# Kernel tuning notes

Hardware: AMD Instinct MI355X
Metric: run time of the kernel (lower is better)

## Reference

```python
import jax, jax.numpy as jnp
import numpy as np

N = 6144
INPUT_SIZE = 1024
HIDDEN = 256
NEG_INF = -9e15  # matches torch masked_fill value -9000000000000000.0


def setup_inputs() -> dict:
    key = jax.random.key(0)
    k1, k2, k3, k4 = jax.random.split(key, 4)
    nodes_embed = jax.random.normal(k1, (N, INPUT_SIZE), dtype=jnp.float32)
    node_adj = jax.random.randint(k2, (N, N), 0, 2, dtype=jnp.int32)
    # learned params (xavier-uniform-ish scaling)
    limW = np.sqrt(6.0 / (INPUT_SIZE + HIDDEN))
    W = jax.random.uniform(k3, (INPUT_SIZE, HIDDEN), minval=-limW, maxval=limW, dtype=jnp.float32)
    lima = 1.414 * np.sqrt(6.0 / (2 * HIDDEN + 1))
    a_edge = jax.random.uniform(k4, (2 * HIDDEN,), minval=-lima, maxval=lima, dtype=jnp.float32)
    return {"nodes_embed": nodes_embed, "W": W, "a_edge": a_edge, "node_adj": node_adj}


def reference(nodes_embed, W, a_edge, node_adj):
    # h = nodes_embed @ W : [N, hidden]
    h = nodes_embed @ W
    # W_edge([h_i ; h_j]) decomposes exactly: (h_i @ a1) + (h_j @ a2)
    a1, a2 = a_edge[:HIDDEN], a_edge[HIDDEN:]
    score = (h @ a1)[:, None] + (h @ a2)[None, :]  # [N, N]
    adj_f = node_adj.astype(h.dtype)
    weight = jax.nn.leaky_relu(adj_f * score, negative_slope=0.2)
    weight = jnp.where(node_adj == 0, jnp.asarray(NEG_INF, h.dtype), weight)
    attention = jax.nn.softmax(weight, axis=-1)
    # dropout in eval mode (identity)
    return attention @ h  # [N, hidden]
```

## Files before the change

### kernel.cpp

```cpp
#include <hip/hip_runtime.h>
#include <hip/hip_bf16.h>

#define NN 6144
#define INPUT 1024
#define HID 256

using frag  = __attribute__((ext_vector_type(8))) short;
using f32x4 = __attribute__((ext_vector_type(4))) float;

static __device__ __forceinline__ unsigned short bf16u(float x) {
    unsigned u = __float_as_uint(x);
    u += 0x7fff + ((u >> 16) & 1);
    return (unsigned short)(u >> 16);
}

static __device__ __forceinline__ void gll16(const void* g, void* l) {
    __builtin_amdgcn_global_load_lds((__attribute__((address_space(1))) const void*)g,
                                     (__attribute__((address_space(3))) void*)l, 16, 0, 0);
}
static __device__ __forceinline__ void gll4(const void* g, void* l) {
    __builtin_amdgcn_global_load_lds((__attribute__((address_space(1))) const void*)g,
                                     (__attribute__((address_space(3))) void*)l, 4, 0, 0);
}

static __device__ __forceinline__ void lds_barrier() {
    asm volatile("s_waitcnt lgkmcnt(0)" ::: "memory");
    __builtin_amdgcn_s_barrier();
    __builtin_amdgcn_sched_barrier(0);
}


__global__ __launch_bounds__(256) void k_prep(const float* __restrict__ X,
                                              const float* __restrict__ W,
                                              unsigned short* __restrict__ Xbp,
                                              unsigned short* __restrict__ Wtp) {
    int b = blockIdx.x;
    if (b < 3072) {
        int t = b * 256 + threadIdx.x;
        int i = t >> 7, k8 = t & 127;
        const float4* p = reinterpret_cast<const float4*>(X + (size_t)i * INPUT + k8 * 8);
        float4 x0 = p[0], x1 = p[1];
        frag v;
        v[0] = (short)bf16u(x0.x); v[1] = (short)bf16u(x0.y);
        v[2] = (short)bf16u(x0.z); v[3] = (short)bf16u(x0.w);
        v[4] = (short)bf16u(x1.x); v[5] = (short)bf16u(x1.y);
        v[6] = (short)bf16u(x1.z); v[7] = (short)bf16u(x1.w);
        size_t off = ((size_t)((i >> 4) * 32 + (k8 >> 2))) * 512 + (k8 & 3) * 128 + (i & 15) * 8;
        *reinterpret_cast<frag*>(Xbp + off) = v;
    } else {
        int u = (b - 3072) * 256 + threadIdx.x;
        int n = u >> 7, k8 = u & 127;
        int k = k8 * 8;
        frag v;
#pragma unroll
        for (int e = 0; e < 8; e++) v[e] = (short)bf16u(W[(size_t)(k + e) * HID + n]);
        size_t off = ((size_t)((n >> 4) * 32 + (k8 >> 2))) * 512 + (k8 & 3) * 128 + (n & 15) * 8;
        *reinterpret_cast<frag*>(Wtp + off) = v;
    }
}

__global__ __launch_bounds__(256, 4) void k_gemm1(const unsigned short* __restrict__ Xbp,
                                                  const unsigned short* __restrict__ Wtp,
                                                  const float* __restrict__ a_edge,
                                                  unsigned short* __restrict__ hTp,
                                                  float* __restrict__ s1,
                                                  float* __restrict__ s2) {
    int t = threadIdx.x;
    int w = t >> 6, l = t & 63, lm = l & 15, q = l >> 4;
    int bx = blockIdx.x, by = blockIdx.y;
    int i0 = bx * 32;
    int tn = by * 4 + w;

    const unsigned short* pA0 = Xbp + (size_t)(bx * 2) * 32 * 512 + l * 8;
    const unsigned short* pA1 = Xbp + (size_t)(bx * 2 + 1) * 32 * 512 + l * 8;
    const unsigned short* pB  = Wtp + (size_t)tn * 32 * 512 + l * 8;

    f32x4 acc0 = {}, acc1 = {};
    frag a0s[3], a1s[3], bs[3];
#pragma unroll
    for (int s = 0; s < 2; s++) {
        a0s[s] = *reinterpret_cast<const frag*>(pA0 + s * 512);
        a1s[s] = *reinterpret_cast<const frag*>(pA1 + s * 512);
        bs[s]  = *reinterpret_cast<const frag*>(pB  + s * 512);
    }
#pragma unroll
    for (int tk = 0; tk < 32; tk++) {
        int cur = tk % 3;
        if (tk < 30) {
            int nx = (tk + 2) % 3;
            a0s[nx] = *reinterpret_cast<const frag*>(pA0 + (tk + 2) * 512);
            a1s[nx] = *reinterpret_cast<const frag*>(pA1 + (tk + 2) * 512);
            bs[nx]  = *reinterpret_cast<const frag*>(pB  + (tk + 2) * 512);
        }
        acc0 = __builtin_amdgcn_mfma_f32_16x16x32_bf16(a0s[cur], bs[cur], acc0, 0, 0, 0);
        acc1 = __builtin_amdgcn_mfma_f32_16x16x32_bf16(a1s[cur], bs[cur], acc1, 0, 0, 0);
    }

    unsigned short* tb = hTp + ((size_t)bx * 16 + tn) * 512;
    ushort4 o;
    o.x = bf16u(acc0[0]); o.y = bf16u(acc0[1]); o.z = bf16u(acc0[2]); o.w = bf16u(acc0[3]);
    *reinterpret_cast<ushort4*>(tb + (q >> 1) * 128 + lm * 8 + (q & 1) * 4) = o;
    o.x = bf16u(acc1[0]); o.y = bf16u(acc1[1]); o.z = bf16u(acc1[2]); o.w = bf16u(acc1[3]);
    *reinterpret_cast<ushort4*>(tb + (2 + (q >> 1)) * 128 + lm * 8 + (q & 1) * 4) = o;

    float a1v = a_edge[tn * 16 + lm], a2v = a_edge[HID + tn * 16 + lm];
#pragma unroll
    for (int h = 0; h < 2; h++) {
        const f32x4& ac = h ? acc1 : acc0;
#pragma unroll
        for (int r = 0; r < 4; r++) {
            float v1 = ac[r] * a1v, v2 = ac[r] * a2v;
            v1 += __shfl_xor(v1, 1); v2 += __shfl_xor(v2, 1);
            v1 += __shfl_xor(v1, 2); v2 += __shfl_xor(v2, 2);
            v1 += __shfl_xor(v1, 4); v2 += __shfl_xor(v2, 4);
            v1 += __shfl_xor(v1, 8); v2 += __shfl_xor(v2, 8);
            if (lm == 0) {
                atomicAdd(&s1[i0 + h * 16 + q * 4 + r], v1);
                atomicAdd(&s2[i0 + h * 16 + q * 4 + r], v2);
            }
        }
    }
}

__global__ __launch_bounds__(512, 2) void k_attn(const int* __restrict__ adj,
                                                 const float* __restrict__ s1,
                                                 const float* __restrict__ s2,
                                                 const unsigned short* __restrict__ hTp,
                                                 float* __restrict__ U4,
                                                 float* __restrict__ denom4) {
    __shared__ unsigned short P[2][32][136];
    __shared__ int   adjS[2][32][128];
    __shared__ float s2S[2][128];
    int t = threadIdx.x;
    int m = t >> 4, cg = t & 15;
    int i0 = blockIdx.x * 32;
    int q4 = blockIdx.y, j0 = q4 * 1536;
    int w = t >> 6, l = t & 63, lm = l & 15, q = l >> 4;

    float s1v = s1[i0 + m];
    const int*   astage = adj + (size_t)(i0 + w * 4 + (l >> 5)) * NN + j0 + (l & 31) * 4;
    const float* sstage = s2 + j0 + w * 16 + l;

    const unsigned short* hb = hTp + (size_t)(w * 2) * 512 + l * 8;
    int tjb = q4 * 48;

    f32x4 acc[2][2] = {};
    float dsum = 0.f;

#define STAGE(JC, BUF) { \
        gll16(astage + (JC), &adjS[BUF][w * 4][0]); \
        gll16(astage + (JC) + 2 * NN, &adjS[BUF][w * 4 + 2][0]); \
        if (l < 16) gll4(sstage + (JC), &s2S[BUF][w * 16]); }

    STAGE(0, 0)

    for (int c = 0; c < 12; c++) {
        int buf = c & 1, jc = c * 128;

        frag bf[8];
#pragma unroll
        for (int kk = 0; kk < 4; kk++)
#pragma unroll
            for (int nt = 0; nt < 2; nt++)
                bf[kk * 2 + nt] = *reinterpret_cast<const frag*>(
                    hb + ((size_t)(tjb + c * 4 + kk) * 16 + nt) * 512);

        asm volatile("s_waitcnt vmcnt(8)" ::: "memory");
        __builtin_amdgcn_s_barrier();
        __builtin_amdgcn_sched_barrier(0);
        if (c < 11) STAGE(jc + 128, buf ^ 1)

        {
            const int*   aL = &adjS[buf][m][cg * 8];
            const float* sL = &s2S[buf][cg * 8];
            int4   av0 = *reinterpret_cast<const int4*>(aL);
            int4   av1 = *reinterpret_cast<const int4*>(aL + 4);
            float4 sv0 = *reinterpret_cast<const float4*>(sL);
            float4 sv1 = *reinterpret_cast<const float4*>(sL + 4);
            float sc, wv, p0, p1, p2, p3, p4, p5, p6, p7;
            sc = s1v + sv0.x; wv = fmaxf(sc, 0.2f * sc); p0 = av0.x ? __expf(wv) : 0.f;
            sc = s1v + sv0.y; wv = fmaxf(sc, 0.2f * sc); p1 = av0.y ? __expf(wv) : 0.f;
            sc = s1v + sv0.z; wv = fmaxf(sc, 0.2f * sc); p2 = av0.z ? __expf(wv) : 0.f;
            sc = s1v + sv0.w; wv = fmaxf(sc, 0.2f * sc); p3 = av0.w ? __expf(wv) : 0.f;
            sc = s1v + sv1.x; wv = fmaxf(sc, 0.2f * sc); p4 = av1.x ? __expf(wv) : 0.f;
            sc = s1v + sv1.y; wv = fmaxf(sc, 0.2f * sc); p5 = av1.y ? __expf(wv) : 0.f;
            sc = s1v + sv1.z; wv = fmaxf(sc, 0.2f * sc); p6 = av1.z ? __expf(wv) : 0.f;
            sc = s1v + sv1.w; wv = fmaxf(sc, 0.2f * sc); p7 = av1.w ? __expf(wv) : 0.f;
            dsum += ((p0 + p1) + (p2 + p3)) + ((p4 + p5) + (p6 + p7));
            frag pk;
            pk[0] = (short)bf16u(p0); pk[1] = (short)bf16u(p1);
            pk[2] = (short)bf16u(p2); pk[3] = (short)bf16u(p3);
            pk[4] = (short)bf16u(p4); pk[5] = (short)bf16u(p5);
            pk[6] = (short)bf16u(p6); pk[7] = (short)bf16u(p7);
            *reinterpret_cast<frag*>(&P[buf][m][cg * 8]) = pk;
        }

        lds_barrier();

        __builtin_amdgcn_s_setprio(1);
#pragma unroll
        for (int kk = 0; kk < 4; kk++) {
            frag a0 = *reinterpret_cast<const frag*>(&P[buf][lm][kk * 32 + q * 8]);
            frag a1 = *reinterpret_cast<const frag*>(&P[buf][16 + lm][kk * 32 + q * 8]);
#pragma unroll
            for (int nt = 0; nt < 2; nt++) {
                acc[0][nt] = __builtin_amdgcn_mfma_f32_16x16x32_bf16(a0, bf[kk * 2 + nt], acc[0][nt], 0, 0, 0);
                acc[1][nt] = __builtin_amdgcn_mfma_f32_16x16x32_bf16(a1, bf[kk * 2 + nt], acc[1][nt], 0, 0, 0);
            }
        }
        __builtin_amdgcn_s_setprio(0);
    }
#undef STAGE

    float v = dsum;
    v += __shfl_xor(v, 1); v += __shfl_xor(v, 2);
    v += __shfl_xor(v, 4); v += __shfl_xor(v, 8);
    if (cg == 0) denom4[(size_t)q4 * NN + i0 + m] = v;

    float* Ub = U4 + (size_t)q4 * NN * HID;
#pragma unroll
    for (int h = 0; h < 2; h++)
#pragma unroll
        for (int nt = 0; nt < 2; nt++)
#pragma unroll
            for (int r = 0; r < 4; r++)
                Ub[(size_t)(i0 + h * 16 + q * 4 + r) * HID + w * 32 + nt * 16 + lm] = acc[h][nt][r];
}

__global__ __launch_bounds__(256) void k_norm(const float* __restrict__ U4,
                                              const float* __restrict__ denom4,
                                              float* __restrict__ out) {
    int i = blockIdx.x, t = threadIdx.x;
    size_t S = (size_t)NN * HID;
    size_t base = (size_t)i * HID + t;
    float u = U4[base] + U4[base + S] + U4[base + 2 * S] + U4[base + 3 * S];
    float d = denom4[i] + denom4[i + NN] + denom4[i + 2 * NN] + denom4[i + 3 * NN];
    out[base] = (d != 0.f) ? u / d : 0.f;
}

extern "C" void kernel_launch(void* const* d_in, const int* in_sizes, int n_in,
                              void* d_out, int out_size, void* d_ws, size_t ws_size,
                              hipStream_t stream) {
    const float* X      = (const float*)d_in[0];
    const float* W      = (const float*)d_in[1];
    const float* a_edge = (const float*)d_in[2];
    const int*   adj    = (const int*)d_in[3];
    float* out = (float*)d_out;

    float* U4     = (float*)d_ws;
    float* denom4 = U4 + (size_t)4 * NN * HID;
    float* s1     = denom4 + (size_t)4 * NN;
    float* s2     = s1 + NN;
    unsigned short* hTp = (unsigned short*)(s2 + NN);
    unsigned short* Wtp = hTp + (size_t)HID * NN;
    unsigned short* Xbp = (unsigned short*)U4;

    hipMemsetAsync(s1, 0, 2 * NN * sizeof(float), stream);
    k_prep<<<3072 + 128, 256, 0, stream>>>(X, W, Xbp, Wtp);
    k_gemm1<<<dim3(NN / 32, 4), 256, 0, stream>>>(Xbp, Wtp, a_edge, hTp, s1, s2);
    k_attn<<<dim3(NN / 32, 4), 512, 0, stream>>>(adj, s1, s2, hTp, U4, denom4);
    k_norm<<<NN, 256, 0, stream>>>(U4, denom4, out);
}
```

Measured before the change: 290.4 us.

## Compute attention probabilities directly in MFMA register fragments, dropping LDS staging

The attention kernel no longer stages adjacency and s2 through LDS or writes P to shared memory. Each lane loads the adjacency and s2 values it needs straight into registers, builds the bf16 B fragment with v_cvt_pk_bf16_f32, and runs the MFMAs with h^T as the A operand. This removes barriers and LDS traffic, and the block shrinks to 256 threads with 3 blocks per CU. Partial outputs are stored in fragment-tiled layout, and the normalization kernel transposes them through LDS and writes float4. The cost is uncoalesced 32-byte adjacency loads per lane with no explicit prefetch pipeline.

```diff
diff --git a/kernel.cpp b/kernel.cpp
--- a/kernel.cpp
+++ b/kernel.cpp
@@ -7,6 +7,8 @@
 
 using frag  = __attribute__((ext_vector_type(8))) short;
 using f32x4 = __attribute__((ext_vector_type(4))) float;
+
+union FU { frag f; unsigned u[4]; };
 
 static __device__ __forceinline__ unsigned short bf16u(float x) {
     unsigned u = __float_as_uint(x);
@@ -14,19 +16,10 @@
     return (unsigned short)(u >> 16);
 }
 
-static __device__ __forceinline__ void gll16(const void* g, void* l) {
-    __builtin_amdgcn_global_load_lds((__attribute__((address_space(1))) const void*)g,
-                                     (__attribute__((address_space(3))) void*)l, 16, 0, 0);
-}
-static __device__ __forceinline__ void gll4(const void* g, void* l) {
-    __builtin_amdgcn_global_load_lds((__attribute__((address_space(1))) const void*)g,
-                                     (__attribute__((address_space(3))) void*)l, 4, 0, 0);
-}
-
-static __device__ __forceinline__ void lds_barrier() {
-    asm volatile("s_waitcnt lgkmcnt(0)" ::: "memory");
-    __builtin_amdgcn_s_barrier();
-    __builtin_amdgcn_sched_barrier(0);
+static __device__ __forceinline__ unsigned cvtpk(float lo, float hi) {
+    unsigned r;
+    asm("v_cvt_pk_bf16_f32 %0, %1, %2" : "=v"(r) : "v"(lo), "v"(hi));
+    return r;
 }
 
 
@@ -122,120 +115,123 @@
     }
 }
 
-__global__ __launch_bounds__(512, 2) void k_attn(const int* __restrict__ adj,
+__global__ __launch_bounds__(256, 3) void k_attn(const int* __restrict__ adj,
                                                  const float* __restrict__ s1,
                                                  const float* __restrict__ s2,
                                                  const unsigned short* __restrict__ hTp,
-                                                 float* __restrict__ U4,
+                                                 float* __restrict__ U4p,
                                                  float* __restrict__ denom4) {
-    __shared__ unsigned short P[2][32][136];
-    __shared__ int   adjS[2][32][128];
-    __shared__ float s2S[2][128];
     int t = threadIdx.x;
-    int m = t >> 4, cg = t & 15;
-    int i0 = blockIdx.x * 32;
+    int w = t >> 6, l = t & 63, lm = l & 15, q = l >> 4;
+    int bx = blockIdx.x, i0 = bx * 32;
     int q4 = blockIdx.y, j0 = q4 * 1536;
-    int w = t >> 6, l = t & 63, lm = l & 15, q = l >> 4;
-
-    float s1v = s1[i0 + m];
-    const int*   astage = adj + (size_t)(i0 + w * 4 + (l >> 5)) * NN + j0 + (l & 31) * 4;
-    const float* sstage = s2 + j0 + w * 16 + l;
-
-    const unsigned short* hb = hTp + (size_t)(w * 2) * 512 + l * 8;
-    int tjb = q4 * 48;
-
-    f32x4 acc[2][2] = {};
-    float dsum = 0.f;
-
-#define STAGE(JC, BUF) { \
-        gll16(astage + (JC), &adjS[BUF][w * 4][0]); \
-        gll16(astage + (JC) + 2 * NN, &adjS[BUF][w * 4 + 2][0]); \
-        if (l < 16) gll4(sstage + (JC), &s2S[BUF][w * 16]); }
-
-    STAGE(0, 0)
-
-    for (int c = 0; c < 12; c++) {
-        int buf = c & 1, jc = c * 128;
-
-        frag bf[8];
-#pragma unroll
-        for (int kk = 0; kk < 4; kk++)
-#pragma unroll
-            for (int nt = 0; nt < 2; nt++)
-                bf[kk * 2 + nt] = *reinterpret_cast<const frag*>(
-                    hb + ((size_t)(tjb + c * 4 + kk) * 16 + nt) * 512);
-
-        asm volatile("s_waitcnt vmcnt(8)" ::: "memory");
-        __builtin_amdgcn_s_barrier();
-        __builtin_amdgcn_sched_barrier(0);
-        if (c < 11) STAGE(jc + 128, buf ^ 1)
-
-        {
-            const int*   aL = &adjS[buf][m][cg * 8];
-            const float* sL = &s2S[buf][cg * 8];
-            int4   av0 = *reinterpret_cast<const int4*>(aL);
-            int4   av1 = *reinterpret_cast<const int4*>(aL + 4);
-            float4 sv0 = *reinterpret_cast<const float4*>(sL);
-            float4 sv1 = *reinterpret_cast<const float4*>(sL + 4);
-            float sc, wv, p0, p1, p2, p3, p4, p5, p6, p7;
-            sc = s1v + sv0.x; wv = fmaxf(sc, 0.2f * sc); p0 = av0.x ? __expf(wv) : 0.f;
-            sc = s1v + sv0.y; wv = fmaxf(sc, 0.2f * sc); p1 = av0.y ? __expf(wv) : 0.f;
-            sc = s1v + sv0.z; wv = fmaxf(sc, 0.2f * sc); p2 = av0.z ? __expf(wv) : 0.f;
-            sc = s1v + sv0.w; wv = fmaxf(sc, 0.2f * sc); p3 = av0.w ? __expf(wv) : 0.f;
-            sc = s1v + sv1.x; wv = fmaxf(sc, 0.2f * sc); p4 = av1.x ? __expf(wv) : 0.f;
-            sc = s1v + sv1.y; wv = fmaxf(sc, 0.2f * sc); p5 = av1.y ? __expf(wv) : 0.f;
-            sc = s1v + sv1.z; wv = fmaxf(sc, 0.2f * sc); p6 = av1.z ? __expf(wv) : 0.f;
-            sc = s1v + sv1.w; wv = fmaxf(sc, 0.2f * sc); p7 = av1.w ? __expf(wv) : 0.f;
-            dsum += ((p0 + p1) + (p2 + p3)) + ((p4 + p5) + (p6 + p7));
-            frag pk;
-            pk[0] = (short)bf16u(p0); pk[1] = (short)bf16u(p1);
-            pk[2] = (short)bf16u(p2); pk[3] = (short)bf16u(p3);
-            pk[4] = (short)bf16u(p4); pk[5] = (short)bf16u(p5);
-            pk[6] = (short)bf16u(p6); pk[7] = (short)bf16u(p7);
-            *reinterpret_cast<frag*>(&P[buf][m][cg * 8]) = pk;
+
+    float s1a = s1[i0 + lm], s1b = s1[i0 + 16 + lm];
+    const int*   aL = adj + (size_t)(i0 + lm) * NN + j0 + q * 8;
+    const int*   aH = aL + (size_t)16 * NN;
+    const float* sp = s2 + j0 + q * 8;
+    const unsigned short* Ab = hTp + ((size_t)(q4 * 48) * 16 + w * 4) * 512 + l * 8;
+
+    f32x4 accL[4] = {}, accH[4] = {};
+    float dsL = 0.f, dsH = 0.f;
+
+#pragma unroll 2
+    for (int st = 0; st < 48; st++) {
+        const unsigned short* Abs = Ab + (size_t)st * 16 * 512;
+        frag A0 = *reinterpret_cast<const frag*>(Abs);
+        frag A1 = *reinterpret_cast<const frag*>(Abs + 512);
+        frag A2 = *reinterpret_cast<const frag*>(Abs + 1024);
+        frag A3 = *reinterpret_cast<const frag*>(Abs + 1536);
+        int4   al0 = *reinterpret_cast<const int4*>(aL + st * 32);
+        int4   al1 = *reinterpret_cast<const int4*>(aL + st * 32 + 4);
+        int4   ah0 = *reinterpret_cast<const int4*>(aH + st * 32);
+        int4   ah1 = *reinterpret_cast<const int4*>(aH + st * 32 + 4);
+        float4 sv0 = *reinterpret_cast<const float4*>(sp + st * 32);
+        float4 sv1 = *reinterpret_cast<const float4*>(sp + st * 32 + 4);
+
+        float sc, wv, p0, p1, p2, p3, p4, p5, p6, p7;
+        FU b0, b1;
+        sc = s1a + sv0.x; wv = fmaxf(sc, 0.2f * sc); p0 = al0.x ? __expf(wv) : 0.f;
+        sc = s1a + sv0.y; wv = fmaxf(sc, 0.2f * sc); p1 = al0.y ? __expf(wv) : 0.f;
+        sc = s1a + sv0.z; wv = fmaxf(sc, 0.2f * sc); p2 = al0.z ? __expf(wv) : 0.f;
+        sc = s1a + sv0.w; wv = fmaxf(sc, 0.2f * sc); p3 = al0.w ? __expf(wv) : 0.f;
+        sc = s1a + sv1.x; wv = fmaxf(sc, 0.2f * sc); p4 = al1.x ? __expf(wv) : 0.f;
+        sc = s1a + sv1.y; wv = fmaxf(sc, 0.2f * sc); p5 = al1.y ? __expf(wv) : 0.f;
+        sc = s1a + sv1.z; wv = fmaxf(sc, 0.2f * sc); p6 = al1.z ? __expf(wv) : 0.f;
+        sc = s1a + sv1.w; wv = fmaxf(sc, 0.2f * sc); p7 = al1.w ? __expf(wv) : 0.f;
+        dsL += ((p0 + p1) + (p2 + p3)) + ((p4 + p5) + (p6 + p7));
+        b0.u[0] = cvtpk(p0, p1); b0.u[1] = cvtpk(p2, p3);
+        b0.u[2] = cvtpk(p4, p5); b0.u[3] = cvtpk(p6, p7);
+        sc = s1b + sv0.x; wv = fmaxf(sc, 0.2f * sc); p0 = ah0.x ? __expf(wv) : 0.f;
+        sc = s1b + sv0.y; wv = fmaxf(sc, 0.2f * sc); p1 = ah0.y ? __expf(wv) : 0.f;
+        sc = s1b + sv0.z; wv = fmaxf(sc, 0.2f * sc); p2 = ah0.z ? __expf(wv) : 0.f;
+        sc = s1b + sv0.w; wv = fmaxf(sc, 0.2f * sc); p3 = ah0.w ? __expf(wv) : 0.f;
+        sc = s1b + sv1.x; wv = fmaxf(sc, 0.2f * sc); p4 = ah1.x ? __expf(wv) : 0.f;
+        sc = s1b + sv1.y; wv = fmaxf(sc, 0.2f * sc); p5 = ah1.y ? __expf(wv) : 0.f;
+        sc = s1b + sv1.z; wv = fmaxf(sc, 0.2f * sc); p6 = ah1.z ? __expf(wv) : 0.f;
+        sc = s1b + sv1.w; wv = fmaxf(sc, 0.2f * sc); p7 = ah1.w ? __expf(wv) : 0.f;
+        dsH += ((p0 + p1) + (p2 + p3)) + ((p4 + p5) + (p6 + p7));
+        b1.u[0] = cvtpk(p0, p1); b1.u[1] = cvtpk(p2, p3);
+        b1.u[2] = cvtpk(p4, p5); b1.u[3] = cvtpk(p6, p7);
+
+        __builtin_amdgcn_s_setprio(1);
+        accL[0] = __builtin_amdgcn_mfma_f32_16x16x32_bf16(A0, b0.f, accL[0], 0, 0, 0);
+        accH[0] = __builtin_amdgcn_mfma_f32_16x16x32_bf16(A0, b1.f, accH[0], 0, 0, 0);
+        accL[1] = __builtin_amdgcn_mfma_f32_16x16x32_bf16(A1, b0.f, accL[1], 0, 0, 0);
+        accH[1] = __builtin_amdgcn_mfma_f32_16x16x32_bf16(A1, b1.f, accH[1], 0, 0, 0);
+        accL[2] = __builtin_amdgcn_mfma_f32_16x16x32_bf16(A2, b0.f, accL[2], 0, 0, 0);
+        accH[2] = __builtin_amdgcn_mfma_f32_16x16x32_bf16(A2, b1.f, accH[2], 0, 0, 0);
+        accL[3] = __builtin_amdgcn_mfma_f32_16x16x32_bf16(A3, b0.f, accL[3], 0, 0, 0);
+        accH[3] = __builtin_amdgcn_mfma_f32_16x16x32_bf16(A3, b1.f, accH[3], 0, 0, 0);
+        __builtin_amdgcn_s_setprio(0);
+    }
+
+    dsL += __shfl_xor(dsL, 16); dsL += __shfl_xor(dsL, 32);
+    dsH += __shfl_xor(dsH, 16); dsH += __shfl_xor(dsH, 32);
+    if (w == 0 && l < 16) {
+        denom4[(size_t)q4 * NN + i0 + l]      = dsL;
+        denom4[(size_t)q4 * NN + i0 + 16 + l] = dsH;
+    }
+
+    float* Ub = U4p + (((size_t)q4 * 192 + bx) * 16) * 512;
+#pragma unroll
+    for (int a = 0; a < 4; a++) {
+        float* tb = Ub + (size_t)(w * 4 + a) * 512;
+#pragma unroll
+        for (int r = 0; r < 4; r++) {
+            tb[(q * 4 + r) * 16 + lm]       = accL[a][r];
+            tb[256 + (q * 4 + r) * 16 + lm] = accH[a][r];
         }
-
-        lds_barrier();
-
-        __builtin_amdgcn_s_setprio(1);
-#pragma unroll
-        for (int kk = 0; kk < 4; kk++) {
-            frag a0 = *reinterpret_cast<const frag*>(&P[buf][lm][kk * 32 + q * 8]);
-            frag a1 = *reinterpret_cast<const frag*>(&P[buf][16 + lm][kk * 32 + q * 8]);
-#pragma unroll
-            for (int nt = 0; nt < 2; nt++) {
-                acc[0][nt] = __builtin_amdgcn_mfma_f32_16x16x32_bf16(a0, bf[kk * 2 + nt], acc[0][nt], 0, 0, 0);
-                acc[1][nt] = __builtin_amdgcn_mfma_f32_16x16x32_bf16(a1, bf[kk * 2 + nt], acc[1][nt], 0, 0, 0);
-            }
-        }
-        __builtin_amdgcn_s_setprio(0);
-    }
-#undef STAGE
-
-    float v = dsum;
-    v += __shfl_xor(v, 1); v += __shfl_xor(v, 2);
-    v += __shfl_xor(v, 4); v += __shfl_xor(v, 8);
-    if (cg == 0) denom4[(size_t)q4 * NN + i0 + m] = v;
-
-    float* Ub = U4 + (size_t)q4 * NN * HID;
-#pragma unroll
-    for (int h = 0; h < 2; h++)
-#pragma unroll
-        for (int nt = 0; nt < 2; nt++)
-#pragma unroll
-            for (int r = 0; r < 4; r++)
-                Ub[(size_t)(i0 + h * 16 + q * 4 + r) * HID + w * 32 + nt * 16 + lm] = acc[h][nt][r];
-}
-
-__global__ __launch_bounds__(256) void k_norm(const float* __restrict__ U4,
+    }
+}
+
+__global__ __launch_bounds__(256) void k_norm(const float* __restrict__ U4p,
                                               const float* __restrict__ denom4,
                                               float* __restrict__ out) {
-    int i = blockIdx.x, t = threadIdx.x;
-    size_t S = (size_t)NN * HID;
-    size_t base = (size_t)i * HID + t;
-    float u = U4[base] + U4[base + S] + U4[base + 2 * S] + U4[base + 3 * S];
-    float d = denom4[i] + denom4[i + NN] + denom4[i + 2 * NN] + denom4[i + 3 * NN];
-    out[base] = (d != 0.f) ? u / d : 0.f;
+    __shared__ float T[32][257];
+    int bx = blockIdx.x, t = threadIdx.x;
+    const float* base = U4p + (size_t)bx * 16 * 512;
+    const size_t QS = (size_t)192 * 16 * 512;
+#pragma unroll
+    for (int e = 0; e < 32; e++) {
+        int f = e * 256 + t;
+        size_t off = (size_t)(f >> 9) * 512 + (f & 511);
+        float u = base[off] + base[QS + off] + base[2 * QS + off] + base[3 * QS + off];
+        int tn = f >> 9, h = (f >> 8) & 1, ns = (f >> 4) & 15, is = f & 15;
+        T[h * 16 + is][tn * 16 + ns] = u;
+    }
+    __syncthreads();
+    int r = t >> 3, c0 = (t & 7) * 32;
+    int i = bx * 32 + r;
+    float d = denom4[i] + denom4[NN + i] + denom4[2 * NN + i] + denom4[3 * NN + i];
+    float inv = (d != 0.f) ? 1.f / d : 0.f;
+#pragma unroll
+    for (int c = c0; c < c0 + 32; c += 4) {
+        float4 v;
+        v.x = T[r][c] * inv; v.y = T[r][c + 1] * inv;
+        v.z = T[r][c + 2] * inv; v.w = T[r][c + 3] * inv;
+        *reinterpret_cast<float4*>(&out[(size_t)i * HID + c]) = v;
+    }
 }
 
 extern "C" void kernel_launch(void* const* d_in, const int* in_sizes, int n_in,
@@ -247,17 +243,17 @@
     const int*   adj    = (const int*)d_in[3];
     float* out = (float*)d_out;
 
-    float* U4     = (float*)d_ws;
-    float* denom4 = U4 + (size_t)4 * NN * HID;
+    float* U4p    = (float*)d_ws;
+    float* denom4 = U4p + (size_t)4 * NN * HID;
     float* s1     = denom4 + (size_t)4 * NN;
     float* s2     = s1 + NN;
     unsigned short* hTp = (unsigned short*)(s2 + NN);
     unsigned short* Wtp = hTp + (size_t)HID * NN;
-    unsigned short* Xbp = (unsigned short*)U4;
+    unsigned short* Xbp = (unsigned short*)U4p;
 
     hipMemsetAsync(s1, 0, 2 * NN * sizeof(float), stream);
     k_prep<<<3072 + 128, 256, 0, stream>>>(X, W, Xbp, Wtp);
     k_gemm1<<<dim3(NN / 32, 4), 256, 0, stream>>>(Xbp, Wtp, a_edge, hTp, s1, s2);
-    k_attn<<<dim3(NN / 32, 4), 512, 0, stream>>>(adj, s1, s2, hTp, U4, denom4);
-    k_norm<<<NN, 256, 0, stream>>>(U4, denom4, out);
-}
+    k_attn<<<dim3(NN / 32, 4), 256, 0, stream>>>(adj, s1, s2, hTp, U4p, denom4);
+    k_norm<<<NN / 32, 256, 0, stream>>>(U4p, denom4, out);
+}
```

New measurement: 344.4 us. 18.6% more time.
